# Kernel optimization log

Hardware: AMD Instinct MI355X
Metric: run time of the kernel (lower is better)

## Reference

```python
import jax, jax.numpy as jnp
import numpy as np

D_IN = 1024
D_ATT = 1024
D_OUT = 1024
N, S = 8, 4096


def setup_inputs() -> dict:
    key = jax.random.key(0)
    ks = jax.random.split(key, 5)
    sc_in = 1.0 / np.sqrt(D_IN)
    sc_att = 1.0 / np.sqrt(D_ATT)
    return {
        "x": jax.random.normal(ks[0], (N, S, D_IN), dtype=jnp.float32),
        "Wq": jax.random.normal(ks[1], (D_IN, D_ATT), dtype=jnp.float32) * sc_in,
        "bq": jnp.zeros((D_ATT,), dtype=jnp.float32),
        "Wk": jax.random.normal(ks[2], (D_IN, D_ATT), dtype=jnp.float32) * sc_in,
        "bk": jnp.zeros((D_ATT,), dtype=jnp.float32),
        "Wv": jax.random.normal(ks[3], (D_IN, D_ATT), dtype=jnp.float32) * sc_in,
        "bv": jnp.zeros((D_ATT,), dtype=jnp.float32),
        "Wo": jax.random.normal(ks[4], (D_ATT, D_OUT), dtype=jnp.float32) * sc_att,
        "bo": jnp.zeros((D_OUT,), dtype=jnp.float32),
    }


def reference(x, Wq, bq, Wk, bk, Wv, bv, Wo, bo):
    # projections: [n, s, h]
    query = jnp.einsum('nsd,dh->nsh', x, Wq) + bq
    keyp = jnp.einsum('nsd,dh->nsh', x, Wk) + bk
    value = jnp.einsum('nsd,dh->nsh', x, Wv) + bv
    fmap = lambda t: jax.nn.elu(t) + 1.0
    Q = fmap(query)
    K = fmap(keyp)
    # per-channel reductions over sequence: [n, h]
    KV = jnp.sum(K * value, axis=1)
    Ksum = jnp.sum(K, axis=1)
    Z = 1.0 / (Q * Ksum[:, None, :] + 1e-6)  # [n, s, h]
    V = Q * KV[:, None, :] * Z  # [n, s, h]
    out = jnp.einsum('nsh,ho->nso', V, Wo) + bo
    return jax.nn.gelu(out)  # flax nn.gelu default approximate=True
```

## Files before the change

kernel.cpp:

```cpp
#include <hip/hip_runtime.h>
#include <hip/hip_bf16.h>

typedef __attribute__((ext_vector_type(8))) short bf16x8;
typedef __attribute__((ext_vector_type(4))) float f32x4;

#define GLOBAL_AS __attribute__((address_space(1)))
#define LDS_AS __attribute__((address_space(3)))

#define DCH 1024
#define SEQ 4096
#define NBATCH 8

static __device__ __forceinline__ unsigned int f2bf(float f) {
    unsigned int u = __float_as_uint(f);
    return (u + 0x7fffu + ((u >> 16) & 1u)) >> 16;
}

static __device__ __forceinline__ void async_copy16(const void* g, void* l) {
    __builtin_amdgcn_global_load_lds((const GLOBAL_AS void*)g, (LDS_AS void*)l, 16, 0, 0);
}

static __device__ __forceinline__ float gelu_tanh(float u) {
    float inner = 0.7978845608028654f * (u + 0.044715f * u * u * u);
    return 0.5f * u * (1.f + tanhf(inner));
}

__global__ __launch_bounds__(256) void cvt_kernel(
    const float4* __restrict__ x, uint4* __restrict__ xb)
{
    size_t t = (size_t)blockIdx.x * 256 + threadIdx.x;
    float4 f0 = x[t * 2], f1 = x[t * 2 + 1];
    uint4 a;
    a.x = f2bf(f0.x) | (f2bf(f0.y) << 16);
    a.y = f2bf(f0.z) | (f2bf(f0.w) << 16);
    a.z = f2bf(f1.x) | (f2bf(f1.y) << 16);
    a.w = f2bf(f1.z) | (f2bf(f1.w) << 16);
    xb[t] = a;
}

__global__ __launch_bounds__(256) void wt_kernel(
    const float* __restrict__ Wk, const float* __restrict__ Wv,
    unsigned short* __restrict__ WkT, unsigned short* __restrict__ WvT)
{
    __shared__ float tile[32][33];
    const float* src = blockIdx.z ? Wv : Wk;
    unsigned short* dst = blockIdx.z ? WvT : WkT;
    int h0 = blockIdx.x * 32, k0 = blockIdx.y * 32;
    int tx = threadIdx.x, ty = threadIdx.y;
#pragma unroll
    for (int i = 0; i < 4; i++)
        tile[ty + i * 8][tx] = src[(size_t)(k0 + ty + i * 8) * DCH + h0 + tx];
    __syncthreads();
#pragma unroll
    for (int i = 0; i < 4; i++)
        dst[(size_t)(h0 + ty + i * 8) * DCH + k0 + tx] =
            (unsigned short)f2bf(tile[tx][ty + i * 8]);
}

__global__ __launch_bounds__(256) void kv_gemm_fast(
    const unsigned short* __restrict__ xb,
    const unsigned short* __restrict__ WkT,
    const unsigned short* __restrict__ WvT,
    const float* __restrict__ bk,
    const float* __restrict__ bv,
    float* __restrict__ part)
{
    __shared__ unsigned short sA[128 * 64];
    __shared__ unsigned short sK[64 * 64];
    __shared__ unsigned short sV[64 * 64];
    __shared__ float red[2][64][2];

    int b = blockIdx.x;
    int r = b & 7, j = b >> 3;
    int h_tile = j & 15;
    int ns = r * 32 + (j >> 4);
    int n = ns >> 5, s_tile = ns & 31;
    int s0 = s_tile * 128, h0 = h_tile * 64;

    int tid = threadIdx.x;
    int lane = tid & 63, wid = tid >> 6;
    int wsg = wid >> 1, wh = wid & 1;
    int col = lane & 15, lhi = lane >> 4;

    const unsigned short* gA[4];
    unsigned short* lA[4];
#pragma unroll
    for (int i = 0; i < 4; i++) {
        int c = (wid * 4 + i) * 64 + lane;
        int row = c >> 3, c8 = (c & 7) ^ (row & 7);
        gA[i] = xb + (size_t)(n * SEQ + s0 + row) * DCH + c8 * 8;
        lA[i] = &sA[(wid * 4 + i) * 512];
    }
    const unsigned short* gK[2];
    const unsigned short* gV[2];
    unsigned short* lK[2];
    unsigned short* lV[2];
#pragma unroll
    for (int i = 0; i < 2; i++) {
        int c = (wid * 2 + i) * 64 + lane;
        int row = c >> 3, c8 = (c & 7) ^ (row & 7);
        gK[i] = WkT + (size_t)(h0 + row) * DCH + c8 * 8;
        gV[i] = WvT + (size_t)(h0 + row) * DCH + c8 * 8;
        lK[i] = &sK[(wid * 2 + i) * 512];
        lV[i] = &sV[(wid * 2 + i) * 512];
    }

    f32x4 acck[4][2], accv[4][2];
#pragma unroll
    for (int mt = 0; mt < 4; mt++)
#pragma unroll
        for (int nt = 0; nt < 2; nt++) {
            acck[mt][nt] = (f32x4){0.f, 0.f, 0.f, 0.f};
            accv[mt][nt] = (f32x4){0.f, 0.f, 0.f, 0.f};
        }

    for (int kk = 0; kk < 16; kk++) {
        int k0 = kk * 64;
#pragma unroll
        for (int i = 0; i < 4; i++) async_copy16(gA[i] + k0, lA[i]);
#pragma unroll
        for (int i = 0; i < 2; i++) async_copy16(gK[i] + k0, lK[i]);
#pragma unroll
        for (int i = 0; i < 2; i++) async_copy16(gV[i] + k0, lV[i]);
        __syncthreads();
#pragma unroll
        for (int ks = 0; ks < 2; ks++) {
            bf16x8 af[4], bkf[2], bvf[2];
            int gg = ks * 4 + lhi;
#pragma unroll
            for (int mt = 0; mt < 4; mt++) {
                int rowa = wsg * 64 + mt * 16 + col;
                af[mt] = *((const bf16x8*)&sA[rowa * 64 + ((gg ^ (rowa & 7)) * 8)]);
            }
#pragma unroll
            for (int nt = 0; nt < 2; nt++) {
                int rowb = wh * 32 + nt * 16 + col;
                int o = rowb * 64 + ((gg ^ (rowb & 7)) * 8);
                bkf[nt] = *((const bf16x8*)&sK[o]);
                bvf[nt] = *((const bf16x8*)&sV[o]);
            }
#pragma unroll
            for (int mt = 0; mt < 4; mt++)
#pragma unroll
                for (int nt = 0; nt < 2; nt++) {
                    acck[mt][nt] = __builtin_amdgcn_mfma_f32_16x16x32_bf16(
                        af[mt], bkf[nt], acck[mt][nt], 0, 0, 0);
                    accv[mt][nt] = __builtin_amdgcn_mfma_f32_16x16x32_bf16(
                        af[mt], bvf[nt], accv[mt][nt], 0, 0, 0);
                }
        }
        __syncthreads();
    }

#pragma unroll
    for (int nt = 0; nt < 2; nt++) {
        int h_local = wh * 32 + nt * 16 + col;
        float bkv = bk[h0 + h_local];
        float bvv = bv[h0 + h_local];
        float pkv = 0.f, pks = 0.f;
#pragma unroll
        for (int mt = 0; mt < 4; mt++)
#pragma unroll
            for (int rr = 0; rr < 4; rr++) {
                float ck = acck[mt][nt][rr] + bkv;
                float cv = accv[mt][nt][rr] + bvv;
                float kq = ck > 0.f ? ck + 1.f : __expf(ck);
                pkv += kq * cv;
                pks += kq;
            }
        pkv += __shfl_xor(pkv, 16);
        pkv += __shfl_xor(pkv, 32);
        pks += __shfl_xor(pks, 16);
        pks += __shfl_xor(pks, 32);
        if (lhi == 0) {
            red[wsg][h_local][0] = pkv;
            red[wsg][h_local][1] = pks;
        }
    }
    __syncthreads();
    if (tid < 128) {
        int h = tid & 63, t = tid >> 6;
        float v = red[0][h][t] + red[1][h][t];
        part[(((size_t)(n * 16 + h_tile) * 2 + t) * 32 + s_tile) * 64 + h] = v;
    }
}

__global__ __launch_bounds__(512) void kv_gemm_slow(
    const float* __restrict__ x,
    const unsigned short* __restrict__ WkT,
    const unsigned short* __restrict__ WvT,
    const float* __restrict__ bk,
    const float* __restrict__ bv,
    float* __restrict__ part)
{
    __shared__ unsigned short sA[128 * 64];
    __shared__ unsigned short sK[128 * 64];
    __shared__ unsigned short sV[128 * 64];
    __shared__ float red[2][128][2];

    int b = blockIdx.x;
    int r = b & 7, j = b >> 3;
    int ns = r * 32 + (j >> 3);
    int h_tile = j & 7;
    int n = ns >> 5, s_tile = ns & 31;
    int s0 = s_tile * 128, h0 = h_tile * 128;

    const float* xA = x + ((size_t)(n * SEQ + s0)) * DCH;

    int tid = threadIdx.x;
    int lane = tid & 63, wid = tid >> 6;
    int wsg = wid >> 2, wh = wid & 3;
    int col = lane & 15, lhi = lane >> 4;

    f32x4 acck[4][2], accv[4][2];
#pragma unroll
    for (int mt = 0; mt < 4; mt++)
#pragma unroll
        for (int nt = 0; nt < 2; nt++) {
            acck[mt][nt] = (f32x4){0.f, 0.f, 0.f, 0.f};
            accv[mt][nt] = (f32x4){0.f, 0.f, 0.f, 0.f};
        }

    for (int kk = 0; kk < 16; kk++) {
        int k0 = kk * 64;
#pragma unroll
        for (int i = 0; i < 2; i++) {
            int c = tid + i * 512;
            int row = c >> 3, c8 = c & 7;
            const float4* p = (const float4*)(xA + (size_t)row * DCH + k0 + c8 * 8);
            float4 f0 = p[0], f1 = p[1];
            unsigned int p0 = f2bf(f0.x) | (f2bf(f0.y) << 16);
            unsigned int p1 = f2bf(f0.z) | (f2bf(f0.w) << 16);
            unsigned int p2 = f2bf(f1.x) | (f2bf(f1.y) << 16);
            unsigned int p3 = f2bf(f1.z) | (f2bf(f1.w) << 16);
            uint4 pk = {p0, p1, p2, p3};
            int g = c8 ^ (row & 7);
            *((uint4*)&sA[row * 64 + g * 8]) = pk;
        }
#pragma unroll
        for (int i = 0; i < 2; i++) {
            int c = tid + i * 512;
            int row = c >> 3, c8 = c & 7;
            int g = c8 ^ (row & 7);
            *((uint4*)&sK[row * 64 + g * 8]) =
                *((const uint4*)(WkT + (size_t)(h0 + row) * DCH + k0 + c8 * 8));
            *((uint4*)&sV[row * 64 + g * 8]) =
                *((const uint4*)(WvT + (size_t)(h0 + row) * DCH + k0 + c8 * 8));
        }
        __syncthreads();
#pragma unroll
        for (int ks = 0; ks < 2; ks++) {
            bf16x8 af[4], bkf[2], bvf[2];
            int gg = ks * 4 + lhi;
#pragma unroll
            for (int mt = 0; mt < 4; mt++) {
                int rowa = wsg * 64 + mt * 16 + col;
                af[mt] = *((const bf16x8*)&sA[rowa * 64 + ((gg ^ (rowa & 7)) * 8)]);
            }
#pragma unroll
            for (int nt = 0; nt < 2; nt++) {
                int rowb = wh * 32 + nt * 16 + col;
                int o = rowb * 64 + ((gg ^ (rowb & 7)) * 8);
                bkf[nt] = *((const bf16x8*)&sK[o]);
                bvf[nt] = *((const bf16x8*)&sV[o]);
            }
#pragma unroll
            for (int mt = 0; mt < 4; mt++)
#pragma unroll
                for (int nt = 0; nt < 2; nt++) {
                    acck[mt][nt] = __builtin_amdgcn_mfma_f32_16x16x32_bf16(
                        af[mt], bkf[nt], acck[mt][nt], 0, 0, 0);
                    accv[mt][nt] = __builtin_amdgcn_mfma_f32_16x16x32_bf16(
                        af[mt], bvf[nt], accv[mt][nt], 0, 0, 0);
                }
        }
        __syncthreads();
    }

#pragma unroll
    for (int nt = 0; nt < 2; nt++) {
        int h_local = wh * 32 + nt * 16 + col;
        float bkv = bk[h0 + h_local];
        float bvv = bv[h0 + h_local];
        float pkv = 0.f, pks = 0.f;
#pragma unroll
        for (int mt = 0; mt < 4; mt++)
#pragma unroll
            for (int rr = 0; rr < 4; rr++) {
                float ck = acck[mt][nt][rr] + bkv;
                float cv = accv[mt][nt][rr] + bvv;
                float kq = ck > 0.f ? ck + 1.f : __expf(ck);
                pkv += kq * cv;
                pks += kq;
            }
        pkv += __shfl_xor(pkv, 16);
        pkv += __shfl_xor(pkv, 32);
        pks += __shfl_xor(pks, 16);
        pks += __shfl_xor(pks, 32);
        if (lhi == 0) {
            red[wsg][h_local][0] = pkv;
            red[wsg][h_local][1] = pks;
        }
    }
    __syncthreads();
    if (tid < 256) {
        int h = tid & 127, t = tid >> 7;
        float v = red[0][h][t] + red[1][h][t];
        int ht = h_tile * 2 + (h >> 6);
        part[(((size_t)(n * 16 + ht) * 2 + t) * 32 + s_tile) * 64 + (h & 63)] = v;
    }
}

__global__ __launch_bounds__(256) void out_part_kernel(
    const float* __restrict__ part, const float* __restrict__ Wo,
    float* __restrict__ part2)
{
    __shared__ float skv[128], sks[128], vs[128];
    int n = blockIdx.x, kc = blockIdx.y, ob = blockIdx.z;
    int tid = threadIdx.x;
    {
        int h = tid & 127, t = tid >> 7;
        int ht = kc * 2 + (h >> 6);
        const float* base = part + (((size_t)(n * 16 + ht) * 2 + t) * 32) * 64;
        float s = 0.f;
#pragma unroll 4
        for (int st = 0; st < 32; st++) s += base[st * 64 + (h & 63)];
        if (t == 0) skv[h] = s; else sks[h] = s;
    }
    __syncthreads();
    if (tid < 128) vs[tid] = skv[tid] / sks[tid];
    __syncthreads();
    int o = ob * 256 + tid;
    float acc = 0.f;
#pragma unroll 8
    for (int k = 0; k < 128; k++)
        acc += vs[k] * Wo[(size_t)(kc * 128 + k) * DCH + o];
    part2[(size_t)(n * 8 + kc) * DCH + o] = acc;
}

__global__ __launch_bounds__(256) void bcast_kernel(
    const float4* __restrict__ part2, const float4* __restrict__ bo,
    float4* __restrict__ out)
{
    int n = blockIdx.x >> 7;
    int sc = blockIdx.x & 127;
    int tid = threadIdx.x;
    float4 a = bo[tid];
#pragma unroll
    for (int kc = 0; kc < 8; kc++) {
        float4 p = part2[(size_t)(n * 8 + kc) * 256 + tid];
        a.x += p.x; a.y += p.y; a.z += p.z; a.w += p.w;
    }
    float4 v;
    v.x = gelu_tanh(a.x);
    v.y = gelu_tanh(a.y);
    v.z = gelu_tanh(a.z);
    v.w = gelu_tanh(a.w);
    size_t base = ((size_t)(n * SEQ) + (size_t)sc * 32) * 256 + tid;
#pragma unroll 4
    for (int s = 0; s < 32; s++)
        out[base + (size_t)s * 256] = v;
}

extern "C" void kernel_launch(void* const* d_in, const int* in_sizes, int n_in,
                              void* d_out, int out_size, void* d_ws, size_t ws_size,
                              hipStream_t stream) {
    const float* x  = (const float*)d_in[0];
    const float* Wk = (const float*)d_in[3];
    const float* bk = (const float*)d_in[4];
    const float* Wv = (const float*)d_in[5];
    const float* bv = (const float*)d_in[6];
    const float* Wo = (const float*)d_in[7];
    const float* bo = (const float*)d_in[8];

    const size_t XB_BYTES = (size_t)NBATCH * SEQ * DCH * 2;
    const size_t TAIL = (4u << 20) + (8u << 20) + (1u << 19);
    bool fast = ws_size >= XB_BYTES + TAIL;

    char* ws = (char*)d_ws;
    unsigned short* xb = (unsigned short*)ws;
    char* base = fast ? ws + XB_BYTES : ws;
    unsigned short* WkT = (unsigned short*)base;
    unsigned short* WvT = WkT + 1024 * 1024;
    float* part  = (float*)(base + 4 * 1024 * 1024);
    float* part2 = part + (size_t)8 * 16 * 2 * 32 * 64;

    wt_kernel<<<dim3(32, 32, 2), dim3(32, 8), 0, stream>>>(Wk, Wv, WkT, WvT);
    if (fast) {
        cvt_kernel<<<16384, 256, 0, stream>>>((const float4*)x, (uint4*)xb);
        kv_gemm_fast<<<4096, 256, 0, stream>>>(xb, WkT, WvT, bk, bv, part);
    } else {
        kv_gemm_slow<<<2048, 512, 0, stream>>>(x, WkT, WvT, bk, bv, part);
    }
    out_part_kernel<<<dim3(8, 8, 4), 256, 0, stream>>>(part, Wo, part2);
    bcast_kernel<<<1024, 256, 0, stream>>>((const float4*)part2, (const float4*)bo,
                                           (float4*)d_out);
}
```

Before: 413.2 us.

## Double-buffer KV GEMM LDS tiles and fuse weight transpose into conversion kernel

The KV projection GEMM now double-buffers its x, Wk and Wv tiles in LDS, so the async global-to-LDS copies for the next K step overlap the MFMA work on the current one, with one barrier per iteration instead of two. MFMA sections are wrapped in s_setprio to favour the math waves, and the reduction scratch reuses the A buffer. The weight transpose is merged into the x-to-bf16 conversion as extra blocks of one launch, removing a kernel launch. The doubled LDS footprint (about 64KB per block) may cut occupancy.

```diff
diff --git a/kernel.cpp b/kernel.cpp
--- a/kernel.cpp
+++ b/kernel.cpp
@@ -25,17 +25,37 @@
     return 0.5f * u * (1.f + tanhf(inner));
 }
 
-__global__ __launch_bounds__(256) void cvt_kernel(
-    const float4* __restrict__ x, uint4* __restrict__ xb)
-{
-    size_t t = (size_t)blockIdx.x * 256 + threadIdx.x;
-    float4 f0 = x[t * 2], f1 = x[t * 2 + 1];
-    uint4 a;
-    a.x = f2bf(f0.x) | (f2bf(f0.y) << 16);
-    a.y = f2bf(f0.z) | (f2bf(f0.w) << 16);
-    a.z = f2bf(f1.x) | (f2bf(f1.y) << 16);
-    a.w = f2bf(f1.z) | (f2bf(f1.w) << 16);
-    xb[t] = a;
+__global__ __launch_bounds__(256) void prep_kernel(
+    const float4* __restrict__ x, uint4* __restrict__ xb,
+    const float* __restrict__ Wk, const float* __restrict__ Wv,
+    unsigned short* __restrict__ WkT, unsigned short* __restrict__ WvT)
+{
+    __shared__ float tile[32][33];
+    int tid = threadIdx.x;
+    if (blockIdx.x < 16384) {
+        size_t t = (size_t)blockIdx.x * 256 + tid;
+        float4 f0 = x[t * 2], f1 = x[t * 2 + 1];
+        uint4 a;
+        a.x = f2bf(f0.x) | (f2bf(f0.y) << 16);
+        a.y = f2bf(f0.z) | (f2bf(f0.w) << 16);
+        a.z = f2bf(f1.x) | (f2bf(f1.y) << 16);
+        a.w = f2bf(f1.z) | (f2bf(f1.w) << 16);
+        xb[t] = a;
+    } else {
+        int b2 = blockIdx.x - 16384;
+        const float* src = (b2 >> 10) ? Wv : Wk;
+        unsigned short* dst = (b2 >> 10) ? WvT : WkT;
+        int h0 = (b2 & 31) * 32, k0 = ((b2 >> 5) & 31) * 32;
+        int tx = tid & 31, ty = tid >> 5;
+#pragma unroll
+        for (int i = 0; i < 4; i++)
+            tile[ty + i * 8][tx] = src[(size_t)(k0 + ty + i * 8) * DCH + h0 + tx];
+        __syncthreads();
+#pragma unroll
+        for (int i = 0; i < 4; i++)
+            dst[(size_t)(h0 + ty + i * 8) * DCH + k0 + tx] =
+                (unsigned short)f2bf(tile[tx][ty + i * 8]);
+    }
 }
 
 __global__ __launch_bounds__(256) void wt_kernel(
@@ -65,10 +85,9 @@
     const float* __restrict__ bv,
     float* __restrict__ part)
 {
-    __shared__ unsigned short sA[128 * 64];
-    __shared__ unsigned short sK[64 * 64];
-    __shared__ unsigned short sV[64 * 64];
-    __shared__ float red[2][64][2];
+    __shared__ __align__(16) unsigned short sA[2][128 * 64];
+    __shared__ __align__(16) unsigned short sK[2][64 * 64];
+    __shared__ __align__(16) unsigned short sV[2][64 * 64];
 
     int b = blockIdx.x;
     int r = b & 7, j = b >> 3;
@@ -83,26 +102,24 @@
     int col = lane & 15, lhi = lane >> 4;
 
     const unsigned short* gA[4];
-    unsigned short* lA[4];
+    int aoff[4];
 #pragma unroll
     for (int i = 0; i < 4; i++) {
         int c = (wid * 4 + i) * 64 + lane;
         int row = c >> 3, c8 = (c & 7) ^ (row & 7);
         gA[i] = xb + (size_t)(n * SEQ + s0 + row) * DCH + c8 * 8;
-        lA[i] = &sA[(wid * 4 + i) * 512];
+        aoff[i] = (wid * 4 + i) * 512;
     }
     const unsigned short* gK[2];
     const unsigned short* gV[2];
-    unsigned short* lK[2];
-    unsigned short* lV[2];
+    int koff[2];
 #pragma unroll
     for (int i = 0; i < 2; i++) {
         int c = (wid * 2 + i) * 64 + lane;
         int row = c >> 3, c8 = (c & 7) ^ (row & 7);
         gK[i] = WkT + (size_t)(h0 + row) * DCH + c8 * 8;
         gV[i] = WvT + (size_t)(h0 + row) * DCH + c8 * 8;
-        lK[i] = &sK[(wid * 2 + i) * 512];
-        lV[i] = &sV[(wid * 2 + i) * 512];
+        koff[i] = (wid * 2 + i) * 512;
     }
 
     f32x4 acck[4][2], accv[4][2];
@@ -114,15 +131,25 @@
             accv[mt][nt] = (f32x4){0.f, 0.f, 0.f, 0.f};
         }
 
+#pragma unroll
+    for (int i = 0; i < 4; i++) async_copy16(gA[i], &sA[0][aoff[i]]);
+#pragma unroll
+    for (int i = 0; i < 2; i++) async_copy16(gK[i], &sK[0][koff[i]]);
+#pragma unroll
+    for (int i = 0; i < 2; i++) async_copy16(gV[i], &sV[0][koff[i]]);
+    __syncthreads();
+
+    int cur = 0;
     for (int kk = 0; kk < 16; kk++) {
-        int k0 = kk * 64;
-#pragma unroll
-        for (int i = 0; i < 4; i++) async_copy16(gA[i] + k0, lA[i]);
-#pragma unroll
-        for (int i = 0; i < 2; i++) async_copy16(gK[i] + k0, lK[i]);
-#pragma unroll
-        for (int i = 0; i < 2; i++) async_copy16(gV[i] + k0, lV[i]);
-        __syncthreads();
+        if (kk < 15) {
+            int k0 = (kk + 1) * 64;
+#pragma unroll
+            for (int i = 0; i < 4; i++) async_copy16(gA[i] + k0, &sA[cur ^ 1][aoff[i]]);
+#pragma unroll
+            for (int i = 0; i < 2; i++) async_copy16(gK[i] + k0, &sK[cur ^ 1][koff[i]]);
+#pragma unroll
+            for (int i = 0; i < 2; i++) async_copy16(gV[i] + k0, &sV[cur ^ 1][koff[i]]);
+        }
 #pragma unroll
         for (int ks = 0; ks < 2; ks++) {
             bf16x8 af[4], bkf[2], bvf[2];
@@ -130,15 +157,16 @@
 #pragma unroll
             for (int mt = 0; mt < 4; mt++) {
                 int rowa = wsg * 64 + mt * 16 + col;
-                af[mt] = *((const bf16x8*)&sA[rowa * 64 + ((gg ^ (rowa & 7)) * 8)]);
+                af[mt] = *((const bf16x8*)&sA[cur][rowa * 64 + ((gg ^ (rowa & 7)) * 8)]);
             }
 #pragma unroll
             for (int nt = 0; nt < 2; nt++) {
                 int rowb = wh * 32 + nt * 16 + col;
                 int o = rowb * 64 + ((gg ^ (rowb & 7)) * 8);
-                bkf[nt] = *((const bf16x8*)&sK[o]);
-                bvf[nt] = *((const bf16x8*)&sV[o]);
-            }
+                bkf[nt] = *((const bf16x8*)&sK[cur][o]);
+                bvf[nt] = *((const bf16x8*)&sV[cur][o]);
+            }
+            __builtin_amdgcn_s_setprio(1);
 #pragma unroll
             for (int mt = 0; mt < 4; mt++)
 #pragma unroll
@@ -148,9 +176,13 @@
                     accv[mt][nt] = __builtin_amdgcn_mfma_f32_16x16x32_bf16(
                         af[mt], bvf[nt], accv[mt][nt], 0, 0, 0);
                 }
+            __builtin_amdgcn_s_setprio(0);
         }
         __syncthreads();
-    }
+        cur ^= 1;
+    }
+
+    float* redf = (float*)&sA[0][0];
 
 #pragma unroll
     for (int nt = 0; nt < 2; nt++) {
@@ -173,14 +205,14 @@
         pks += __shfl_xor(pks, 16);
         pks += __shfl_xor(pks, 32);
         if (lhi == 0) {
-            red[wsg][h_local][0] = pkv;
-            red[wsg][h_local][1] = pks;
+            redf[(wsg * 64 + h_local) * 2 + 0] = pkv;
+            redf[(wsg * 64 + h_local) * 2 + 1] = pks;
         }
     }
     __syncthreads();
     if (tid < 128) {
         int h = tid & 63, t = tid >> 6;
-        float v = red[0][h][t] + red[1][h][t];
+        float v = redf[(h) * 2 + t] + redf[(64 + h) * 2 + t];
         part[(((size_t)(n * 16 + h_tile) * 2 + t) * 32 + s_tile) * 64 + h] = v;
     }
 }
@@ -385,11 +417,12 @@
     float* part  = (float*)(base + 4 * 1024 * 1024);
     float* part2 = part + (size_t)8 * 16 * 2 * 32 * 64;
 
-    wt_kernel<<<dim3(32, 32, 2), dim3(32, 8), 0, stream>>>(Wk, Wv, WkT, WvT);
     if (fast) {
-        cvt_kernel<<<16384, 256, 0, stream>>>((const float4*)x, (uint4*)xb);
+        prep_kernel<<<18432, 256, 0, stream>>>((const float4*)x, (uint4*)xb,
+                                               Wk, Wv, WkT, WvT);
         kv_gemm_fast<<<4096, 256, 0, stream>>>(xb, WkT, WvT, bk, bv, part);
     } else {
+        wt_kernel<<<dim3(32, 32, 2), dim3(32, 8), 0, stream>>>(Wk, Wv, WkT, WvT);
         kv_gemm_slow<<<2048, 512, 0, stream>>>(x, WkT, WvT, bk, bv, part);
     }
     out_part_kernel<<<dim3(8, 8, 4), 256, 0, stream>>>(part, Wo, part2);
```

Result: slower. 432.0 us (+4.6%).
